# Optimization experiments

Measured on AMD Instinct MI355X. Metric: run time of the kernel, lower is better.

The kernel has to match this reference:

```python
import jax, jax.numpy as jnp
from jax import lax
import numpy as np

KERNEL_SIZE = 5
GROUP_SIZE = 40
GMAX = 160                      # g sampled in [0, GMAX)
MAX_ITERS = (GMAX - 1) // GROUP_SIZE   # static upper bound on |g|//group_size = 3
B = 4096
D = 8192


def _circ_conv(x, k):
    # x: [1, B, D], k: [B, K] -> grouped (depthwise) circular conv1d, groups=B
    pad = KERNEL_SIZE - 1
    left = pad // 2
    xp = jnp.pad(x, ((0, 0), (0, 0), (left, pad - left)), mode='wrap')
    return lax.conv_general_dilated(
        xp, k[:, None, :], window_strides=(1,), padding='VALID',
        feature_group_count=k.shape[0], dimension_numbers=('NCH', 'OIH', 'NCH'))


def setup_inputs() -> dict:
    key = jax.random.key(0)
    k1, k2, k3 = jax.random.split(key, 3)
    x = jax.random.normal(k1, (B, D), dtype=jnp.float32)
    g = jax.random.randint(k2, (B,), 0, GMAX, dtype=jnp.int32)
    kernels = jax.random.normal(k3, (2 * GROUP_SIZE + 1, KERNEL_SIZE), dtype=jnp.float32)
    return {"x": x, "g": g, "kernels": kernels}


def reference(x, g, kernels):
    G = GROUP_SIZE
    xc = x[None]                          # [1, B, D]  (x.view(-1,1,D).permute(1,0,2))
    sign = jnp.sign(g)                    # [B]
    iters = jnp.abs(g) // G               # [B] data-dependent per-sample loop count
    max_it = jnp.max(iters)               # dynamic max over the batch
    max_k = kernels[sign * G + G]         # [B, K]
    id_k = kernels[G]                     # [K] learned 'identity' kernel
    # true delta kernel: exact no-op under circular pad, used for steps past max_it
    delta = jnp.zeros((KERNEL_SIZE,), x.dtype).at[(KERNEL_SIZE - 1) // 2].set(1.0)

    h = xc
    for i in range(MAX_ITERS):            # static bound; delta makes extra steps no-ops
        inactive = jnp.where(i < max_it, id_k, delta)          # [K]
        k_i = jnp.where((i < iters)[:, None], max_k, inactive[None, :])  # [B, K]
        h = _circ_conv(h, k_i)
    rem = jnp.abs(g) % G
    fin_k = kernels[rem * sign + G]       # [B, K]
    out = _circ_conv(h, fin_k)            # [1, B, D]
    return jnp.transpose(out, (1, 0, 2))  # [B, 1, D]
```

## Files before the change

kernel.cpp:

```cpp
#include <hip/hip_runtime.h>

#define BB 4096
#define DD 8192
#define KK 5
#define GS 40
#define MAXIT 3
#define EFF 17
#define D4 (DD/4)

__global__ __launch_bounds__(256) void k_max_it(const int* __restrict__ g,
                                                int* __restrict__ ws) {
    __shared__ int red[256];
    int t = threadIdx.x;
    int m = 0;
    for (int i = t; i < BB; i += 256) {
        int a = g[i];
        a = a < 0 ? -a : a;
        m = max(m, a / GS);
    }
    red[t] = m;
    __syncthreads();
    for (int s = 128; s > 0; s >>= 1) {
        if (t < s) red[t] = max(red[t], red[t + s]);
        __syncthreads();
    }
    if (t == 0) ws[0] = red[0];
}

__global__ __launch_bounds__(256) void k_conv(const float* __restrict__ x,
                                              const int* __restrict__ g,
                                              const float* __restrict__ kernels,
                                              const int* __restrict__ ws,
                                              float* __restrict__ out) {
    __shared__ float row[DD];
    const int b = blockIdx.x;
    const int t = threadIdx.x;

    const float4* xr = (const float4*)(x + (size_t)b * DD);
    float4* rowv = (float4*)row;
#pragma unroll
    for (int i = 0; i < D4 / 256; ++i)
        rowv[i * 256 + t] = xr[i * 256 + t];

    const int gv = g[b];
    const int sign = gv > 0 ? 1 : (gv < 0 ? -1 : 0);
    const int a = gv < 0 ? -gv : gv;
    const int iters = a / GS;
    const int rem = a % GS;
    const int max_it = ws[0];

    float maxk[KK], idk[KK], fink[KK];
    const float* mk = kernels + (size_t)(sign * GS + GS) * KK;
    const float* ik = kernels + (size_t)GS * KK;
    const float* fk = kernels + (size_t)(rem * sign + GS) * KK;
#pragma unroll
    for (int j = 0; j < KK; ++j) { maxk[j] = mk[j]; idk[j] = ik[j]; fink[j] = fk[j]; }

    float e[EFF], ne[EFF];
#pragma unroll
    for (int m = 0; m < EFF; ++m) e[m] = 0.f;
    e[0] = 1.f;
    int len = 1;
    for (int i = 0; i < MAXIT; ++i) {
        float kk5[KK];
        if (i < iters) {
#pragma unroll
            for (int j = 0; j < KK; ++j) kk5[j] = maxk[j];
        } else if (i < max_it) {
#pragma unroll
            for (int j = 0; j < KK; ++j) kk5[j] = idk[j];
        } else {
#pragma unroll
            for (int j = 0; j < KK; ++j) kk5[j] = (j == (KK - 1) / 2) ? 1.f : 0.f;
        }
#pragma unroll
        for (int m = 0; m < EFF; ++m) ne[m] = 0.f;
        for (int m = 0; m < len; ++m)
#pragma unroll
            for (int j = 0; j < KK; ++j) ne[m + j] += e[m] * kk5[j];
        len += KK - 1;
#pragma unroll
        for (int m = 0; m < EFF; ++m) e[m] = ne[m];
    }
#pragma unroll
    for (int m = 0; m < EFF; ++m) ne[m] = 0.f;
    for (int m = 0; m < len; ++m)
#pragma unroll
        for (int j = 0; j < KK; ++j) ne[m + j] += e[m] * fink[j];
#pragma unroll
    for (int m = 0; m < EFF; ++m) e[m] = ne[m];

    __syncthreads();

    float4* outr = (float4*)(out + (size_t)b * DD);
#pragma unroll
    for (int jb = 0; jb < D4 / 256; ++jb) {
        const int v = jb * 256 + t;
        float f[EFF + 3];
#pragma unroll
        for (int q = 0; q < 5; ++q) {
            unsigned idx = (unsigned)(v - 2 + q) & (D4 - 1);
            float4 val = rowv[idx];
            f[q * 4 + 0] = val.x; f[q * 4 + 1] = val.y;
            f[q * 4 + 2] = val.z; f[q * 4 + 3] = val.w;
        }
        float oc[4];
#pragma unroll
        for (int c = 0; c < 4; ++c) {
            float s = 0.f;
#pragma unroll
            for (int m = 0; m < EFF; ++m) s += e[m] * f[c + m];
            oc[c] = s;
        }
        float4 o; o.x = oc[0]; o.y = oc[1]; o.z = oc[2]; o.w = oc[3];
        outr[v] = o;
    }
}

extern "C" void kernel_launch(void* const* d_in, const int* in_sizes, int n_in,
                              void* d_out, int out_size, void* d_ws, size_t ws_size,
                              hipStream_t stream) {
    const float* x       = (const float*)d_in[0];
    const int*   g       = (const int*)d_in[1];
    const float* kernels = (const float*)d_in[2];
    float*       out     = (float*)d_out;
    int*         ws      = (int*)d_ws;

    k_max_it<<<1, 256, 0, stream>>>(g, ws);
    k_conv<<<BB, 256, 0, stream>>>(x, g, kernels, ws, out);
}
```

Measured before the change: 240.1 us.

## Fuse max-iteration reduction into conv kernel, drop LDS staging, use nontemporal stores

The separate single-block reduction kernel is removed. Each wavefront of the conv kernel now recomputes the batch-wide max of |g| from a vectorized read of g plus a shuffle reduction. The row is no longer staged in shared memory; the stencil reads neighbouring float4s straight from global memory and relies on cache hits, and outputs use nontemporal stores. This saves a launch and the LDS round trip, at the cost of every block redundantly reading all of g and making 5x overlapping global loads.

```diff
diff --git a/kernel.cpp b/kernel.cpp
--- a/kernel.cpp
+++ b/kernel.cpp
@@ -8,46 +8,35 @@
 #define EFF 17
 #define D4 (DD/4)
 
-__global__ __launch_bounds__(256) void k_max_it(const int* __restrict__ g,
-                                                int* __restrict__ ws) {
-    __shared__ int red[256];
-    int t = threadIdx.x;
-    int m = 0;
-    for (int i = t; i < BB; i += 256) {
-        int a = g[i];
-        a = a < 0 ? -a : a;
-        m = max(m, a / GS);
+typedef float vf4 __attribute__((ext_vector_type(4)));
+
+__device__ __forceinline__ int iabs(int a) { return a < 0 ? -a : a; }
+
+__global__ __launch_bounds__(256) void k_fused(const float* __restrict__ x,
+                                               const int* __restrict__ g,
+                                               const float* __restrict__ kernels,
+                                               float* __restrict__ out) {
+    const int b    = blockIdx.x;
+    const int t    = threadIdx.x;
+    const int lane = t & 63;
+
+    const int4* g4 = (const int4*)g;
+    int gm = 0;
+#pragma unroll
+    for (int i = 0; i < 16; ++i) {
+        int4 v = g4[lane + 64 * i];
+        gm = max(gm, max(max(iabs(v.x), iabs(v.y)), max(iabs(v.z), iabs(v.w))));
     }
-    red[t] = m;
-    __syncthreads();
-    for (int s = 128; s > 0; s >>= 1) {
-        if (t < s) red[t] = max(red[t], red[t + s]);
-        __syncthreads();
-    }
-    if (t == 0) ws[0] = red[0];
-}
+#pragma unroll
+    for (int off = 32; off > 0; off >>= 1)
+        gm = max(gm, __shfl_xor(gm, off));
+    const int max_it = gm / GS;
 
-__global__ __launch_bounds__(256) void k_conv(const float* __restrict__ x,
-                                              const int* __restrict__ g,
-                                              const float* __restrict__ kernels,
-                                              const int* __restrict__ ws,
-                                              float* __restrict__ out) {
-    __shared__ float row[DD];
-    const int b = blockIdx.x;
-    const int t = threadIdx.x;
-
-    const float4* xr = (const float4*)(x + (size_t)b * DD);
-    float4* rowv = (float4*)row;
-#pragma unroll
-    for (int i = 0; i < D4 / 256; ++i)
-        rowv[i * 256 + t] = xr[i * 256 + t];
-
-    const int gv = g[b];
-    const int sign = gv > 0 ? 1 : (gv < 0 ? -1 : 0);
-    const int a = gv < 0 ? -gv : gv;
+    const int gv    = g[b];
+    const int sign  = gv > 0 ? 1 : (gv < 0 ? -1 : 0);
+    const int a     = iabs(gv);
     const int iters = a / GS;
-    const int rem = a % GS;
-    const int max_it = ws[0];
+    const int rem   = a % GS;
 
     float maxk[KK], idk[KK], fink[KK];
     const float* mk = kernels + (size_t)(sign * GS + GS) * KK;
@@ -90,9 +79,8 @@
 #pragma unroll
     for (int m = 0; m < EFF; ++m) e[m] = ne[m];
 
-    __syncthreads();
-
-    float4* outr = (float4*)(out + (size_t)b * DD);
+    const float4* xr   = (const float4*)(x + (size_t)b * DD);
+    vf4*          outr = (vf4*)(out + (size_t)b * DD);
 #pragma unroll
     for (int jb = 0; jb < D4 / 256; ++jb) {
         const int v = jb * 256 + t;
@@ -100,7 +88,7 @@
 #pragma unroll
         for (int q = 0; q < 5; ++q) {
             unsigned idx = (unsigned)(v - 2 + q) & (D4 - 1);
-            float4 val = rowv[idx];
+            float4 val = xr[idx];
             f[q * 4 + 0] = val.x; f[q * 4 + 1] = val.y;
             f[q * 4 + 2] = val.z; f[q * 4 + 3] = val.w;
         }
@@ -112,8 +100,9 @@
             for (int m = 0; m < EFF; ++m) s += e[m] * f[c + m];
             oc[c] = s;
         }
-        float4 o; o.x = oc[0]; o.y = oc[1]; o.z = oc[2]; o.w = oc[3];
-        outr[v] = o;
+        vf4 o;
+        o.x = oc[0]; o.y = oc[1]; o.z = oc[2]; o.w = oc[3];
+        __builtin_nontemporal_store(o, outr + v);
     }
 }
 
@@ -124,8 +113,6 @@
     const int*   g       = (const int*)d_in[1];
     const float* kernels = (const float*)d_in[2];
     float*       out     = (float*)d_out;
-    int*         ws      = (int*)d_ws;
 
-    k_max_it<<<1, 256, 0, stream>>>(g, ws);
-    k_conv<<<BB, 256, 0, stream>>>(x, g, kernels, ws, out);
+    k_fused<<<BB, 256, 0, stream>>>(x, g, kernels, out);
 }
```

After: 281.2 us. 17.1% more time.

## Split each row into four chunks with halos and use nontemporal stores

Applied to the files above, without the earlier changes.

Each block now handles a 2048-element chunk of a row instead of the full row. Halo float4s are loaded so the circular wrap is handled at load time rather than by masking indices. This quadruples the grid and cuts LDS use per block from 32KB to about 8KB, which should raise occupancy and latency hiding. Output is written with nontemporal stores to avoid polluting cache, at the cost of recomputing the effective kernel four times per row and a small redundant halo read. The max-iteration reduction also moves the divide out of the loop.

```diff
diff --git a/kernel.cpp b/kernel.cpp
--- a/kernel.cpp
+++ b/kernel.cpp
@@ -6,25 +6,27 @@
 #define GS 40
 #define MAXIT 3
 #define EFF 17
-#define D4 (DD/4)
+#define CHUNK 2048
+#define C4 (CHUNK/4)
+#define DF4 (DD/4)
+
+typedef float vf4 __attribute__((ext_vector_type(4)));
+
+__device__ __forceinline__ int iabs(int a) { return a < 0 ? -a : a; }
 
 __global__ __launch_bounds__(256) void k_max_it(const int* __restrict__ g,
                                                 int* __restrict__ ws) {
     __shared__ int red[256];
     int t = threadIdx.x;
     int m = 0;
-    for (int i = t; i < BB; i += 256) {
-        int a = g[i];
-        a = a < 0 ? -a : a;
-        m = max(m, a / GS);
-    }
+    for (int i = t; i < BB; i += 256) m = max(m, iabs(g[i]));
     red[t] = m;
     __syncthreads();
     for (int s = 128; s > 0; s >>= 1) {
         if (t < s) red[t] = max(red[t], red[t + s]);
         __syncthreads();
     }
-    if (t == 0) ws[0] = red[0];
+    if (t == 0) ws[0] = red[0] / GS;
 }
 
 __global__ __launch_bounds__(256) void k_conv(const float* __restrict__ x,
@@ -32,21 +34,32 @@
                                               const float* __restrict__ kernels,
                                               const int* __restrict__ ws,
                                               float* __restrict__ out) {
-    __shared__ float row[DD];
-    const int b = blockIdx.x;
-    const int t = threadIdx.x;
+    __shared__ float lds[CHUNK + 16];
+    float4* ldsv = (float4*)lds;
+
+    const int bi   = blockIdx.x;
+    const int b    = bi >> 2;
+    const int ch   = bi & 3;
+    const int t    = threadIdx.x;
+    const int c0f4 = ch * C4;
 
     const float4* xr = (const float4*)(x + (size_t)b * DD);
-    float4* rowv = (float4*)row;
-#pragma unroll
-    for (int i = 0; i < D4 / 256; ++i)
-        rowv[i * 256 + t] = xr[i * 256 + t];
 
-    const int gv = g[b];
-    const int sign = gv > 0 ? 1 : (gv < 0 ? -1 : 0);
-    const int a = gv < 0 ? -gv : gv;
+    ldsv[2 + t]       = xr[c0f4 + t];
+    ldsv[2 + t + 256] = xr[c0f4 + t + 256];
+    if (t == 0) {
+        ldsv[0] = xr[(c0f4 - 2) & (DF4 - 1)];
+        ldsv[1] = xr[(c0f4 - 1) & (DF4 - 1)];
+    } else if (t == 1) {
+        ldsv[514] = xr[(c0f4 + C4)     & (DF4 - 1)];
+        ldsv[515] = xr[(c0f4 + C4 + 1) & (DF4 - 1)];
+    }
+
+    const int gv    = g[b];
+    const int sign  = gv > 0 ? 1 : (gv < 0 ? -1 : 0);
+    const int a     = iabs(gv);
     const int iters = a / GS;
-    const int rem = a % GS;
+    const int rem   = a % GS;
     const int max_it = ws[0];
 
     float maxk[KK], idk[KK], fink[KK];
@@ -92,15 +105,14 @@
 
     __syncthreads();
 
-    float4* outr = (float4*)(out + (size_t)b * DD);
+    vf4* outr = (vf4*)(out + (size_t)b * DD);
 #pragma unroll
-    for (int jb = 0; jb < D4 / 256; ++jb) {
+    for (int jb = 0; jb < 2; ++jb) {
         const int v = jb * 256 + t;
         float f[EFF + 3];
 #pragma unroll
         for (int q = 0; q < 5; ++q) {
-            unsigned idx = (unsigned)(v - 2 + q) & (D4 - 1);
-            float4 val = rowv[idx];
+            float4 val = ldsv[v + q];
             f[q * 4 + 0] = val.x; f[q * 4 + 1] = val.y;
             f[q * 4 + 2] = val.z; f[q * 4 + 3] = val.w;
         }
@@ -112,8 +124,9 @@
             for (int m = 0; m < EFF; ++m) s += e[m] * f[c + m];
             oc[c] = s;
         }
-        float4 o; o.x = oc[0]; o.y = oc[1]; o.z = oc[2]; o.w = oc[3];
-        outr[v] = o;
+        vf4 o;
+        o.x = oc[0]; o.y = oc[1]; o.z = oc[2]; o.w = oc[3];
+        __builtin_nontemporal_store(o, outr + c0f4 + v);
     }
 }
 
@@ -127,5 +140,5 @@
     int*         ws      = (int*)d_ws;
 
     k_max_it<<<1, 256, 0, stream>>>(g, ws);
-    k_conv<<<BB, 256, 0, stream>>>(x, g, kernels, ws, out);
+    k_conv<<<BB * (DD / CHUNK), 256, 0, stream>>>(x, g, kernels, ws, out);
 }
```

Result: no change. 236.7 us (-1.4%).
